# Performance work log

Hardware: AMD Instinct MI355X
Metric: run time of the kernel (lower is better)

## Reference

```python
import jax, jax.numpy as jnp
import numpy as np

N_NODES = 100000


def setup_inputs() -> dict:
    key = jax.random.key(0)
    k1, k2, k3, k4 = jax.random.split(key, 4)
    d = 128
    R = 3
    E = 500000
    h = jax.random.normal(k1, (N_NODES, d), dtype=jnp.float32)
    # per-relation bias-free linear weights, scaled ~1/sqrt(d_in)
    W = jax.random.normal(k2, (R, d, d), dtype=jnp.float32) * (1.0 / np.sqrt(d))
    src = jax.random.randint(k3, (R, E), 0, N_NODES, dtype=jnp.int32)
    dst = jax.random.randint(k4, (R, E), 0, N_NODES, dtype=jnp.int32)
    return {"h": h, "W": W, "src": src, "dst": dst}


def reference(h, W, src, dst):
    # h: [N, d_in], W: [R, d_in, d_out], src/dst: [R, E]
    N = h.shape[0]
    # Transform node features per relation first (cheaper: N < E), then gather per edge.
    hW = jnp.einsum('nd,rdo->rno', h, W)                      # [R, N, d_out]
    msgs = jax.vmap(lambda t, s: t[s])(hW, src)               # [R, E, d_out] gather
    # segment-mean over each node's incoming edges (mailbox mean), per relation
    sums = jax.vmap(lambda m, d_: jax.ops.segment_sum(m, d_, num_segments=N))(msgs, dst)  # [R, N, d_out]
    cnts = jax.vmap(lambda d_: jax.ops.segment_sum(jnp.ones(d_.shape, jnp.float32), d_, num_segments=N))(dst)  # [R, N]
    mean_msgs = sums / jnp.maximum(cnts, 1.0)[..., None]      # [R, N, d_out]
    # reduce_f: mailbox mean + residual node feature, then cross-relation mean
    h_per_rel = mean_msgs + h[None, :, :]                     # [R, N, d_out]
    return jnp.mean(h_per_rel, axis=0)                        # [N, d_out]
```

## Files before the change

kernel.cpp:

```cpp
#include <hip/hip_runtime.h>

#define D 128
#define TN 64
#define NR 3
#define PAD 16
#define NBSH 10
#define BCAP 1024
#define SCAP 4096
#define BSTRIDE (8 * BCAP + SCAP)
#define NBK 293
#define EPB 4096
#define CPOOL 65536

typedef short short8 __attribute__((ext_vector_type(8)));
typedef float f32x4 __attribute__((ext_vector_type(4)));
typedef float f32x2 __attribute__((ext_vector_type(2)));

__device__ __forceinline__ unsigned int f2bf(float x) {
    unsigned int u = __float_as_uint(x);
    return (u + 0x7fffu + ((u >> 16) & 1u)) >> 16;
}

__global__ __launch_bounds__(256) void prep_bin_k(
    const float* __restrict__ h, unsigned char* __restrict__ h8,
    unsigned short* __restrict__ hb, const float* __restrict__ W,
    unsigned short* __restrict__ Wb, const int* __restrict__ src,
    const int* __restrict__ dst, int* __restrict__ gcur, int* __restrict__ buf,
    int n8, int n8tot, int nbConv, int E, int N, int RE) {
    int bid = blockIdx.x;
    int tid = threadIdx.x;
    if (bid < nbConv) {
        int i = bid * 256 + tid;
        if (i >= n8tot) return;
        if (i >= n8) {
            ((uint2*)h8)[i] = make_uint2(0u, 0u);
            ((uint4*)hb)[i] = make_uint4(0u, 0u, 0u, 0u);
            return;
        }
        const float4* hp = (const float4*)h;
        float4 v0 = hp[2 * i + 0], v1 = hp[2 * i + 1];
        int w0 = __builtin_amdgcn_cvt_pk_fp8_f32(v0.x, v0.y, 0, false);
        w0 = __builtin_amdgcn_cvt_pk_fp8_f32(v0.z, v0.w, w0, true);
        int w1 = __builtin_amdgcn_cvt_pk_fp8_f32(v1.x, v1.y, 0, false);
        w1 = __builtin_amdgcn_cvt_pk_fp8_f32(v1.z, v1.w, w1, true);
        ((uint2*)h8)[i] = make_uint2((unsigned)w0, (unsigned)w1);
        uint4 o;
        o.x = f2bf(v0.x) | (f2bf(v0.y) << 16);
        o.y = f2bf(v0.z) | (f2bf(v0.w) << 16);
        o.z = f2bf(v1.x) | (f2bf(v1.y) << 16);
        o.w = f2bf(v1.z) | (f2bf(v1.w) << 16);
        ((uint4*)hb)[i] = o;
        return;
    }
    bid -= nbConv;
    if (bid < 24) {
        int t = bid * 256 + tid;
        if (t >= 12 * 8 * 64) return;
        int lane = t & 63, cg = (t >> 6) & 7, kg = t >> 9;
        int col = cg * 16 + (lane & 15);
        int r = kg >> 2;
        int klocal = (kg & 3) * 32 + (lane >> 4) * 8;
        const float* Ws = W + ((size_t)r * D + klocal) * D + col;
        uint4 o;
        o.x = f2bf(Ws[0 * D]) | (f2bf(Ws[1 * D]) << 16);
        o.y = f2bf(Ws[2 * D]) | (f2bf(Ws[3 * D]) << 16);
        o.z = f2bf(Ws[4 * D]) | (f2bf(Ws[5 * D]) << 16);
        o.w = f2bf(Ws[6 * D]) | (f2bf(Ws[7 * D]) << 16);
        ((uint4*)Wb)[t] = o;
        return;
    }
    bid -= 24;
    __shared__ int hist[NBK];
    __shared__ int bas[NBK];
    int base = bid * EPB;
    int E2 = 2 * E;
    int pk[16], bk[16];
#pragma unroll
    for (int j = 0; j < 16; ++j) {
        int idx = base + j * 256 + tid;
        if (idx < RE) {
            int r = (idx >= E2) ? 2 : ((idx >= E) ? 1 : 0);
            int d = dst[idx];
            int s = src[idx];
            int rn = r * N + d;
            bk[j] = rn >> NBSH;
            pk[j] = (s << NBSH) | (rn & (BCAP - 1));
        } else {
            bk[j] = -1;
            pk[j] = 0;
        }
    }
    for (int i = tid; i < NBK; i += 256) hist[i] = 0;
    __syncthreads();
#pragma unroll
    for (int j = 0; j < 16; ++j)
        if (bk[j] >= 0) atomicAdd(&hist[bk[j]], 1);
    __syncthreads();
    int sh = bid & 7;
    for (int b = tid; b < NBK; b += 256) {
        int c = hist[b];
        bas[b] = (c > 0) ? atomicAdd(&gcur[b * 9 + sh], c) : 0;
        hist[b] = 0;
    }
    __syncthreads();
#pragma unroll
    for (int j = 0; j < 16; ++j) {
        if (bk[j] < 0) continue;
        int b = bk[j];
        int l = atomicAdd(&hist[b], 1);
        int slot = bas[b] + l;
        if (slot < BCAP) {
            buf[(size_t)b * BSTRIDE + sh * BCAP + slot] = pk[j];
        } else {
            int sp = atomicAdd(&gcur[b * 9 + 8], 1);
            if (sp < SCAP) buf[(size_t)b * BSTRIDE + 8 * BCAP + sp] = pk[j];
        }
    }
}

__global__ __launch_bounds__(256) void scatter_k(
    const int* __restrict__ gcur, const int* __restrict__ buf,
    int* __restrict__ csr, int* __restrict__ deg, int* __restrict__ ovfh,
    int2* __restrict__ chain, int* __restrict__ ccnt, int RN) {
    int b = blockIdx.x, tid = threadIdx.x;
    __shared__ int cur[BCAP];
    for (int i = tid; i < BCAP; i += 256) cur[i] = 0;
    __syncthreads();
    int rn0 = b << NBSH;
    for (int sh = 0; sh < 9; ++sh) {
        int len = gcur[b * 9 + sh];
        int cap = (sh < 8) ? BCAP : SCAP;
        if (len > cap) len = cap;
        int off = (int)((size_t)b * BSTRIDE) + ((sh < 8) ? sh * BCAP : 8 * BCAP);
        for (int i = tid; i < len; i += 256) {
            int pk = buf[off + i];
            int rnl = pk & (BCAP - 1);
            int s = ((unsigned)pk) >> NBSH;
            int pos = atomicAdd(&cur[rnl], 1);
            int rn = rn0 + rnl;
            if (pos < PAD) {
                csr[((size_t)rn << 4) + pos] = s;
            } else {
                int ci = atomicAdd(ccnt, 1);
                if (ci < CPOOL) {
                    int old = atomicExch(&ovfh[rn], ci);
                    chain[ci] = make_int2(s, old);
                }
            }
        }
    }
    __syncthreads();
    for (int i = tid; i < BCAP; i += 256) {
        int rn = rn0 + i;
        if (rn < RN) deg[rn] = cur[i];
    }
}

__global__ __launch_bounds__(512) void fused_k(
    const unsigned char* __restrict__ h8, const unsigned short* __restrict__ hb,
    const int* __restrict__ csr, const int* __restrict__ deg,
    const int* __restrict__ ovfh, const int2* __restrict__ chain,
    const unsigned short* __restrict__ Wb, float* __restrict__ out, int N) {
    __shared__ uint4 Ald[4 * 4 * 64];
    __shared__ int ilist[NR][PAD][TN];
    __shared__ int degs_s[NR][TN];

    const int tid = threadIdx.x;
    const int blk = blockIdx.x;

    for (int i = tid; i < NR * TN * (PAD / 4); i += 512) {
        int jv = i & 3;
        int nl = (i >> 2) & (TN - 1);
        int r = i >> 8;
        int n = blk * TN + nl;
        if (n >= N) n = N - 1;
        int4 v = ((const int4*)(csr + ((size_t)(r * N + n) << 4)))[jv];
        ilist[r][jv * 4 + 0][nl] = v.x;
        ilist[r][jv * 4 + 1][nl] = v.y;
        ilist[r][jv * 4 + 2][nl] = v.z;
        ilist[r][jv * 4 + 3][nl] = v.w;
    }
    if (tid < NR * TN) {
        int r = tid / TN, nl = tid - r * TN;
        int n = blk * TN + nl;
        if (n >= N) n = N - 1;
        degs_s[r][nl] = deg[r * N + n];
    }
    __syncthreads();

    const int lane = tid & 63;
    const int nl = tid >> 3;
    const int fb = tid & 7;
    const int w = tid >> 6;
    const int wr = w >> 2, wc = w & 3;
    int n_node = blk * TN + nl;
    if (n_node >= N) n_node = N - 1;

    const short8* Ap = (const short8*)Ald;
    const short8* Bp = (const short8*)Wb;
    f32x4 acc[2][2];
#pragma unroll
    for (int m = 0; m < 2; ++m)
#pragma unroll
        for (int n = 0; n < 2; ++n) acc[m][n] = (f32x4){0.f, 0.f, 0.f, 0.f};

#define CVT(x, hi) __builtin_amdgcn_cvt_pk_f32_fp8((int)(x), hi)
#define ACC16(u)                                                             \
    {                                                                        \
        b0 += CVT((u).x, false); b1 += CVT((u).x, true);                     \
        b2 += CVT((u).y, false); b3 += CVT((u).y, true);                     \
        b4 += CVT((u).z, false); b5 += CVT((u).z, true);                     \
        b6 += CVT((u).w, false); b7 += CVT((u).w, true);                     \
    }
#define GLD(s) (*(const uint4*)(h8 + ((size_t)(s) << 7) + fb * 16))

    for (int r = 0; r < NR; ++r) {
        int cr = degs_s[r][nl];
        f32x2 b0 = {0.f, 0.f}, b1 = {0.f, 0.f}, b2 = {0.f, 0.f},
              b3 = {0.f, 0.f}, b4 = {0.f, 0.f}, b5 = {0.f, 0.f},
              b6 = {0.f, 0.f}, b7 = {0.f, 0.f};
        {
            int s0 = (0 < cr) ? ilist[r][0][nl] : N;
            int s1 = (1 < cr) ? ilist[r][1][nl] : N;
            int s2 = (2 < cr) ? ilist[r][2][nl] : N;
            int s3 = (3 < cr) ? ilist[r][3][nl] : N;
            int s4 = (4 < cr) ? ilist[r][4][nl] : N;
            int s5 = (5 < cr) ? ilist[r][5][nl] : N;
            int s6 = (6 < cr) ? ilist[r][6][nl] : N;
            int s7 = (7 < cr) ? ilist[r][7][nl] : N;
            uint4 u0 = GLD(s0), u1 = GLD(s1), u2 = GLD(s2), u3 = GLD(s3);
            uint4 u4 = GLD(s4), u5 = GLD(s5), u6 = GLD(s6), u7 = GLD(s7);
            ACC16(u0); ACC16(u1); ACC16(u2); ACC16(u3);
            ACC16(u4); ACC16(u5); ACC16(u6); ACC16(u7);
        }
        if (cr > 8) {
            int s0 = (8 < cr) ? ilist[r][8][nl] : N;
            int s1 = (9 < cr) ? ilist[r][9][nl] : N;
            int s2 = (10 < cr) ? ilist[r][10][nl] : N;
            int s3 = (11 < cr) ? ilist[r][11][nl] : N;
            int s4 = (12 < cr) ? ilist[r][12][nl] : N;
            int s5 = (13 < cr) ? ilist[r][13][nl] : N;
            int s6 = (14 < cr) ? ilist[r][14][nl] : N;
            int s7 = (15 < cr) ? ilist[r][15][nl] : N;
            uint4 u0 = GLD(s0), u1 = GLD(s1), u2 = GLD(s2), u3 = GLD(s3);
            uint4 u4 = GLD(s4), u5 = GLD(s5), u6 = GLD(s6), u7 = GLD(s7);
            ACC16(u0); ACC16(u1); ACC16(u2); ACC16(u3);
            ACC16(u4); ACC16(u5); ACC16(u6); ACC16(u7);
            if (cr > PAD) {
                int e = ovfh[r * N + n_node];
                while (e >= 0) {
                    int2 ce = chain[e];
                    uint4 uu = GLD(ce.x);
                    ACC16(uu);
                    e = ce.y;
                }
            }
        }
        float sc = 1.0f / (3.0f * fmaxf((float)cr, 1.0f));
        int abase = (((nl >> 4) << 2) + (fb >> 1)) * 64 + (nl & 15);
        uint4 o;
        o.x = f2bf(b0.x * sc) | (f2bf(b0.y * sc) << 16);
        o.y = f2bf(b1.x * sc) | (f2bf(b1.y * sc) << 16);
        o.z = f2bf(b2.x * sc) | (f2bf(b2.y * sc) << 16);
        o.w = f2bf(b3.x * sc) | (f2bf(b3.y * sc) << 16);
        Ald[abase + ((fb & 1) * 2 + 0) * 16] = o;
        o.x = f2bf(b4.x * sc) | (f2bf(b4.y * sc) << 16);
        o.y = f2bf(b5.x * sc) | (f2bf(b5.y * sc) << 16);
        o.z = f2bf(b6.x * sc) | (f2bf(b6.y * sc) << 16);
        o.w = f2bf(b7.x * sc) | (f2bf(b7.y * sc) << 16);
        Ald[abase + ((fb & 1) * 2 + 1) * 16] = o;
        __syncthreads();

#pragma unroll
        for (int kg = 0; kg < 4; ++kg) {
            short8 a[2], b[2];
#pragma unroll
            for (int m = 0; m < 2; ++m)
                a[m] = Ap[(((wr * 2 + m) << 2) + kg) * 64 + lane];
#pragma unroll
            for (int n = 0; n < 2; ++n)
                b[n] = Bp[(((size_t)(r * 4 + kg) * 8) + wc * 2 + n) * 64 + lane];
#pragma unroll
            for (int m = 0; m < 2; ++m)
#pragma unroll
                for (int n = 0; n < 2; ++n)
                    acc[m][n] = __builtin_amdgcn_mfma_f32_16x16x32_bf16(
                        a[m], b[n], acc[m][n], 0, 0, 0);
        }
        __syncthreads();
    }
#undef CVT
#undef ACC16
#undef GLD

    int col0 = wc * 32 + (lane & 15);
    int rloc = wr * 32 + ((lane >> 4) << 2);
#pragma unroll
    for (int m = 0; m < 2; ++m)
#pragma unroll
        for (int rr = 0; rr < 4; ++rr) {
            int row = blk * TN + rloc + m * 16 + rr;
            if (row < N) {
                const unsigned short* ap = hb + ((size_t)row << 7) + col0;
                float* op = out + ((size_t)row << 7) + col0;
#pragma unroll
                for (int n = 0; n < 2; ++n)
                    op[n * 16] =
                        __uint_as_float((unsigned int)ap[n * 16] << 16) +
                        acc[m][n][rr];
            }
        }
}

extern "C" void kernel_launch(void* const* d_in, const int* in_sizes, int n_in,
                              void* d_out, int out_size, void* d_ws, size_t ws_size,
                              hipStream_t stream) {
    const float* h = (const float*)d_in[0];
    const float* W = (const float*)d_in[1];
    const int* src = (const int*)d_in[2];
    const int* dst = (const int*)d_in[3];
    float* out = (float*)d_out;

    const int N = in_sizes[0] / D;
    const int E = in_sizes[2] / NR;
    const int RN = NR * N;
    const int RE = NR * E;
    const int nBuckets = (RN + BCAP - 1) >> NBSH;

    auto al16 = [](size_t x) { return (x + 15) & ~(size_t)15; };
    size_t sz_h8 = al16((size_t)(N + 1) * D);
    size_t sz_hb = al16((size_t)(N + 1) * D * 2);
    size_t sz_Wb = al16((size_t)12 * 8 * 64 * 8 * 2);
    size_t sz_gcur = al16((size_t)nBuckets * 9 * 4);
    size_t sz_buf = al16((size_t)nBuckets * BSTRIDE * 4);
    size_t sz_csr = al16((size_t)RN * PAD * 4);
    size_t sz_deg = al16((size_t)RN * 4);
    size_t sz_ovfh = al16((size_t)RN * 4);
    size_t sz_ccnt = al16(16);
    size_t sz_chain = al16((size_t)CPOOL * 8);

    char* p = (char*)d_ws;
    unsigned char*  h8 = (unsigned char*)p;  p += sz_h8;
    unsigned short* hb = (unsigned short*)p; p += sz_hb;
    unsigned short* Wb = (unsigned short*)p; p += sz_Wb;
    int*  gcur  = (int*)p; p += sz_gcur;
    int*  buf   = (int*)p; p += sz_buf;
    int*  csr   = (int*)p; p += sz_csr;
    int*  deg   = (int*)p; p += sz_deg;
    int*  ovfh  = (int*)p; p += sz_ovfh;
    int*  ccnt  = (int*)p; p += sz_ccnt;
    int2* chain = (int2*)p; p += sz_chain;

    hipMemsetAsync(gcur, 0, (size_t)nBuckets * 9 * 4, stream);
    hipMemsetAsync(ovfh, 0xFF, (size_t)RN * 4, stream);
    hipMemsetAsync(ccnt, 0, 4, stream);

    int n8 = N * D / 8, n8tot = (N + 1) * D / 8;
    int nbConv = (n8tot + 255) / 256;
    int nbBin = (RE + EPB - 1) / EPB;
    prep_bin_k<<<nbConv + 24 + nbBin, 256, 0, stream>>>(
        h, h8, hb, W, Wb, src, dst, gcur, buf, n8, n8tot, nbConv, E, N, RE);
    scatter_k<<<nBuckets, 256, 0, stream>>>(gcur, buf, csr, deg, ovfh, chain,
                                            ccnt, RN);

    int nb = (N + TN - 1) / TN;
    fused_k<<<nb, 512, 0, stream>>>(h8, hb, csr, deg, ovfh, chain, Wb, out, N);
}
```

Measured before the change: 128.7 us.

## Shrink per-node CSR padding to 12 and flatten scatter loop over sub-buckets

Cuts the fixed per-node neighbor slots from 16 to 12, which shrinks CSR storage and the ilist staging loads and drops four gather slots in the fused kernel. Average in-degree is about 5, so more nodes spill into the overflow chain, but chains stay rare. The scatter kernel now runs 512 threads over one flattened prefix-summed range covering all sub-buckets instead of looping over each sub-bucket. It also initializes ovfh itself, removing a separate memset. A single shared ccnt atomic still handles the extra overflow entries, and nodes beyond 12 edges take the slower pointer-chasing path.

```diff
diff --git a/kernel.cpp b/kernel.cpp
--- a/kernel.cpp
+++ b/kernel.cpp
@@ -3,7 +3,7 @@
 #define D 128
 #define TN 64
 #define NR 3
-#define PAD 16
+#define PAD 12
 #define NBSH 10
 #define BCAP 1024
 #define SCAP 4096
@@ -118,39 +118,55 @@
     }
 }
 
-__global__ __launch_bounds__(256) void scatter_k(
+__global__ __launch_bounds__(512) void scatter_k(
     const int* __restrict__ gcur, const int* __restrict__ buf,
     int* __restrict__ csr, int* __restrict__ deg, int* __restrict__ ovfh,
     int2* __restrict__ chain, int* __restrict__ ccnt, int RN) {
     int b = blockIdx.x, tid = threadIdx.x;
     __shared__ int cur[BCAP];
-    for (int i = tid; i < BCAP; i += 256) cur[i] = 0;
-    __syncthreads();
+    __shared__ int pref[10];
+    __shared__ int offs[9];
     int rn0 = b << NBSH;
-    for (int sh = 0; sh < 9; ++sh) {
-        int len = gcur[b * 9 + sh];
-        int cap = (sh < 8) ? BCAP : SCAP;
-        if (len > cap) len = cap;
-        int off = (int)((size_t)b * BSTRIDE) + ((sh < 8) ? sh * BCAP : 8 * BCAP);
-        for (int i = tid; i < len; i += 256) {
-            int pk = buf[off + i];
-            int rnl = pk & (BCAP - 1);
-            int s = ((unsigned)pk) >> NBSH;
-            int pos = atomicAdd(&cur[rnl], 1);
-            int rn = rn0 + rnl;
-            if (pos < PAD) {
-                csr[((size_t)rn << 4) + pos] = s;
-            } else {
-                int ci = atomicAdd(ccnt, 1);
-                if (ci < CPOOL) {
-                    int old = atomicExch(&ovfh[rn], ci);
-                    chain[ci] = make_int2(s, old);
-                }
+    for (int i = tid; i < BCAP; i += 512) {
+        cur[i] = 0;
+        int rn = rn0 + i;
+        if (rn < RN) ovfh[rn] = -1;
+    }
+    if (tid == 0) {
+        int acc = 0;
+        for (int s = 0; s < 9; ++s) {
+            int len = gcur[b * 9 + s];
+            int cap = (s < 8) ? BCAP : SCAP;
+            if (len > cap) len = cap;
+            pref[s] = acc;
+            acc += len;
+            offs[s] = (s < 8) ? s * BCAP : 8 * BCAP;
+        }
+        pref[9] = acc;
+    }
+    __syncthreads();
+    int total = pref[9];
+    for (int g = tid; g < total; g += 512) {
+        int sh = 0;
+        while (sh < 8 && g >= pref[sh + 1]) ++sh;
+        int i = g - pref[sh];
+        int pk = buf[(size_t)b * BSTRIDE + offs[sh] + i];
+        int rnl = pk & (BCAP - 1);
+        int s = ((unsigned)pk) >> NBSH;
+        int pos = atomicAdd(&cur[rnl], 1);
+        int rn = rn0 + rnl;
+        if (pos < PAD) {
+            csr[(size_t)rn * PAD + pos] = s;
+        } else {
+            int ci = atomicAdd(ccnt, 1);
+            if (ci < CPOOL) {
+                int old = atomicExch(&ovfh[rn], ci);
+                chain[ci] = make_int2(s, old);
             }
         }
     }
     __syncthreads();
-    for (int i = tid; i < BCAP; i += 256) {
+    for (int i = tid; i < BCAP; i += 512) {
         int rn = rn0 + i;
         if (rn < RN) deg[rn] = cur[i];
     }
@@ -169,12 +185,13 @@
     const int blk = blockIdx.x;
 
     for (int i = tid; i < NR * TN * (PAD / 4); i += 512) {
-        int jv = i & 3;
-        int nl = (i >> 2) & (TN - 1);
-        int r = i >> 8;
+        int jv = i % 3;
+        int t = i / 3;
+        int nl = t & (TN - 1);
+        int r = t >> 6;
         int n = blk * TN + nl;
         if (n >= N) n = N - 1;
-        int4 v = ((const int4*)(csr + ((size_t)(r * N + n) << 4)))[jv];
+        int4 v = ((const int4*)(csr + (size_t)(r * N + n) * PAD))[jv];
         ilist[r][jv * 4 + 0][nl] = v.x;
         ilist[r][jv * 4 + 1][nl] = v.y;
         ilist[r][jv * 4 + 2][nl] = v.z;
@@ -238,14 +255,8 @@
             int s1 = (9 < cr) ? ilist[r][9][nl] : N;
             int s2 = (10 < cr) ? ilist[r][10][nl] : N;
             int s3 = (11 < cr) ? ilist[r][11][nl] : N;
-            int s4 = (12 < cr) ? ilist[r][12][nl] : N;
-            int s5 = (13 < cr) ? ilist[r][13][nl] : N;
-            int s6 = (14 < cr) ? ilist[r][14][nl] : N;
-            int s7 = (15 < cr) ? ilist[r][15][nl] : N;
             uint4 u0 = GLD(s0), u1 = GLD(s1), u2 = GLD(s2), u3 = GLD(s3);
-            uint4 u4 = GLD(s4), u5 = GLD(s5), u6 = GLD(s6), u7 = GLD(s7);
             ACC16(u0); ACC16(u1); ACC16(u2); ACC16(u3);
-            ACC16(u4); ACC16(u5); ACC16(u6); ACC16(u7);
             if (cr > PAD) {
                 int e = ovfh[r * N + n_node];
                 while (e >= 0) {
@@ -352,7 +363,6 @@
     int2* chain = (int2*)p; p += sz_chain;
 
     hipMemsetAsync(gcur, 0, (size_t)nBuckets * 9 * 4, stream);
-    hipMemsetAsync(ovfh, 0xFF, (size_t)RN * 4, stream);
     hipMemsetAsync(ccnt, 0, 4, stream);
 
     int n8 = N * D / 8, n8tot = (N + 1) * D / 8;
@@ -360,7 +370,7 @@
     int nbBin = (RE + EPB - 1) / EPB;
     prep_bin_k<<<nbConv + 24 + nbBin, 256, 0, stream>>>(
         h, h8, hb, W, Wb, src, dst, gcur, buf, n8, n8tot, nbConv, E, N, RE);
-    scatter_k<<<nBuckets, 256, 0, stream>>>(gcur, buf, csr, deg, ovfh, chain,
+    scatter_k<<<nBuckets, 512, 0, stream>>>(gcur, buf, csr, deg, ovfh, chain,
                                             ccnt, RN);
 
     int nb = (N + TN - 1) / TN;
```

Result: faster. 123.0 us (-4.4%).
